# Optimization experiments

Hardware: AMD Instinct MI355X
Metric: run time of the kernel (lower is better)

Reference implementation:

```python
import jax, jax.numpy as jnp
import numpy as np

K = 12  # nsample_k; graph per point has K nodes (self + K-1 abs-diff neighbors)


def setup_inputs() -> dict:
    key = jax.random.key(0)
    k1, k2, k3 = jax.random.split(key, 3)
    p = jax.random.normal(k1, (2, 8192, 3), dtype=jnp.float32)
    W = jax.random.normal(k2, (1, 3), dtype=jnp.float32) * 0.5  # GCNConv lin weight [out=1, in=3]
    b = jax.random.normal(k3, (1,), dtype=jnp.float32) * 0.1    # GCNConv bias
    return {"p": p, "W": W, "b": b}


def _knn_idx(pts, k):
    # k nearest neighbors over the whole flattened cloud, self included then dropped
    pts = jax.lax.stop_gradient(pts)  # indices are non-differentiable
    sq = jnp.sum(pts * pts, axis=-1)                      # [n]
    d2 = sq[:, None] + sq[None, :] - 2.0 * (pts @ pts.T)  # [n, n] squared distances
    _, idx = jax.lax.top_k(-d2, k)                        # ascending distance
    return idx[:, 1:]                                     # drop self -> [n, k-1]


def reference(p, W, b):
    # p: [B, N, 3] -> flatten to [n, 3]
    pts = p.reshape(-1, 3)
    nidx = _knn_idx(pts, K)            # [n, K-1]
    nbr = pts[nidx]                    # [n, K-1, 3]
    # node features of each star graph: node 0 = point, nodes 1..K-1 = |p - neighbor|
    p_ij = jnp.concatenate([pts[:, None, :], jnp.abs(pts[:, None, :] - nbr)], axis=1)  # [n, K, 3]
    # GCNConv(3,1) on identical star graphs (edges 0->j, plus self loops), closed form:
    #   deg0 = 1, deg_j = 2  =>  out0 = x0 W^T + b ; out_j = x0 W^T / sqrt(2) + x_j W^T / 2 + b
    xw = jnp.einsum('nkc,oc->nko', p_ij, W)  # [n, K, 1]
    inv_s2 = 1.0 / jnp.sqrt(jnp.float32(2.0))
    out0 = xw[:, :1] + b                                  # [n, 1, 1]
    outj = inv_s2 * xw[:, :1] + 0.5 * xw[:, 1:] + b       # [n, K-1, 1]
    emb = jnp.concatenate([out0, outj], axis=1)           # [n, K, 1]
    # POOL: squeeze -> [n, K]; AdaptiveAvgPool1d(1) -> [n, 1]; module returns avg only
    return jnp.mean(emb[..., 0], axis=1, keepdims=True)   # [n, 1]
```

## Files before the change

### kernel.cpp

```cpp
#include <hip/hip_runtime.h>
#include <math.h>


#define NBINS  2048
#define PARTS  16
#define CMIN_  (-6.0f)
#define INVBW_ ((float)NBINS / 12.0f)
#define BLOCK  256
#define WPB    4
#define SEED   768
#define KK     12
#define CD     4
#define BIG    3.0e38f

__device__ __forceinline__ int bin_of(float x) {
  int b = (int)((x - CMIN_) * INVBW_);
  b = b < 0 ? 0 : b;
  b = b > NBINS - 1 ? NBINS - 1 : b;
  return b;
}

__device__ __forceinline__ float wave_min(float v) {
#pragma unroll
  for (int o = 1; o < 64; o <<= 1) v = fminf(v, __shfl_xor(v, o));
  return v;
}

__device__ __forceinline__ void ins4(float (&qd)[CD], float (&qw)[CD],
                                     float d, float w) {
#pragma unroll
  for (int k = CD - 1; k >= 1; --k) {
    const bool up  = (qd[k - 1] > d);
    const bool mid = (qd[k] > d);
    const float nd = up ? qd[k - 1] : (mid ? d : qd[k]);
    const float nw = up ? qw[k - 1] : (mid ? w : qw[k]);
    qd[k] = nd; qw[k] = nw;
  }
  if (qd[0] > d) { qw[0] = w; qd[0] = d; }
}

__global__ __launch_bounds__(1024)
void sort_kernel(const float* __restrict__ p, int* __restrict__ c_all,
                 float4* __restrict__ s_all, int n) {
  __shared__ int h_all[NBINS];
  __shared__ int h_pre[NBINS];
  __shared__ int wsum[16];
  const int tid  = threadIdx.x;
  const int dim  = blockIdx.x / PARTS;
  const int part = blockIdx.x % PARTS;
  const int chunk   = (n + PARTS - 1) / PARTS;
  const int myStart = part * chunk;
  const int myEnd   = min(myStart + chunk, n);

  h_all[tid] = 0; h_all[tid + 1024] = 0;
  h_pre[tid] = 0; h_pre[tid + 1024] = 0;
  __syncthreads();

  for (int i = tid; i < n; i += 1024) {
    const int b = bin_of(p[3 * i + dim]);
    atomicAdd(&h_all[b], 1);
    if (i < myStart) atomicAdd(&h_pre[b], 1);
  }
  __syncthreads();

  const int a = h_all[2 * tid], b = h_all[2 * tid + 1];
  const int v = a + b;
  const int lane = tid & 63, wid = tid >> 6;
  int incl = v;
#pragma unroll
  for (int o = 1; o < 64; o <<= 1) {
    const int t = __shfl_up(incl, o);
    if (lane >= o) incl += t;
  }
  if (lane == 63) wsum[wid] = incl;
  __syncthreads();
  int woff = 0;
  for (int wI = 0; wI < wid; ++wI) woff += wsum[wI];
  const int excl = woff + incl - v;

  if (part == 0) {
    int* __restrict__ cursor = c_all + (size_t)dim * NBINS;
    cursor[2 * tid]     = excl + a;
    cursor[2 * tid + 1] = excl + a + b;
  }

  const int c0 = excl + h_pre[2 * tid];
  const int c1 = excl + a + h_pre[2 * tid + 1];
  __syncthreads();
  h_pre[2 * tid]     = c0;
  h_pre[2 * tid + 1] = c1;
  __syncthreads();

  float4* __restrict__ sorted = s_all + (size_t)dim * n;
  for (int i = myStart + tid; i < myEnd; i += 1024) {
    const float x = p[3 * i], y = p[3 * i + 1], z = p[3 * i + 2];
    const float c = (dim == 0) ? x : (dim == 1) ? y : z;
    const int pos = atomicAdd(&h_pre[bin_of(c)], 1);
    sorted[pos] = make_float4(x, y, z, __int_as_float(i));
  }
}

__global__ __launch_bounds__(BLOCK, 1)
void query_kernel(const float4* __restrict__ sx, const float4* __restrict__ sy,
                  const float4* __restrict__ sz, const int* __restrict__ cx,
                  const int* __restrict__ cy, const int* __restrict__ cz,
                  const float* __restrict__ W, const float* __restrict__ bias,
                  float* __restrict__ out, int n) {
  const int lane = threadIdx.x & 63;
  const int wv   = threadIdx.x >> 6;
  const int t    = wv * (n >> 2) + blockIdx.x;
  const float W0 = W[0], W1 = W[1], W2 = W[2];
  const float bb = bias[0];

  const float4 me = sx[t];
  const float xi = me.x, yi = me.y, zi = me.z;
  const int orig = __float_as_int(me.w);

  const float ax = fabsf(xi), ay = fabsf(yi), az = fabsf(zi);
  const float4* sv; const int* cur; float cq;
  if (ay >= ax && ay >= az)      { sv = sy; cur = cy; cq = yi; }
  else if (az >= ax && az >= ay) { sv = sz; cur = cz; cq = zi; }
  else                           { sv = sx; cur = cx; cq = xi; }

  const int bq = bin_of(cq);
  const int bs = (bq > 0) ? cur[bq - 1] : 0;
  const int be = cur[bq];
  int lo = ((bs + be) >> 1) - SEED / 2;
  lo = lo < 0 ? 0 : lo;
  lo = lo > n - SEED ? n - SEED : lo;
  const float4* base = sv + lo + lane;

  float qd[CD], qw[CD];
  float ev = BIG;
#pragma unroll
  for (int k = 0; k < CD; ++k) { qd[k] = BIG; qw[k] = 0.f; }

#define PROCQ(cc, valid)                                                      \
  {                                                                           \
    const float dx = xi - (cc).x, dy = yi - (cc).y, dz = zi - (cc).z;         \
    float d2 = fmaf(dx, dx, fmaf(dy, dy, dz * dz));                           \
    d2 = (valid) ? d2 : BIG;                                                  \
    const float w = fmaf(W0, fabsf(dx), fmaf(W1, fabsf(dy), W2 * fabsf(dz))); \
    ev = fminf(ev, fmaxf(d2, qd[CD - 1]));                                    \
    ins4(qd, qw, d2, w);                                                      \
  }

  {
    float4 cs[SEED / 64];
#pragma unroll
    for (int s = 0; s < SEED / 64; ++s) cs[s] = base[s * 64];
    __builtin_amdgcn_sched_barrier(0);
#pragma unroll
    for (int s = 0; s < SEED / 64; ++s) PROCQ(cs[s], true)
  }

  float u;
  {
    const float m = qd[0];
    float hiv = m;
#pragma unroll
    for (int o = 1; o < 64; o <<= 1) hiv = fmaxf(hiv, __shfl_xor(hiv, o));
    float lov = 0.f;
#pragma unroll
    for (int it = 0; it < 10; ++it) {
      const float mid = 0.5f * (lov + hiv);
      const int cnt = __popcll(__ballot(m <= mid));
      if (cnt >= KK) hiv = mid; else lov = mid;
    }
    u = hiv;
  }

  const float s = sqrtf(u);
  const int bl = bin_of(cq - s);
  const int bh = bin_of(cq + s);
  const int lo2 = (bl > 0) ? cur[bl - 1] : 0;
  const int hi2 = cur[bh];
  const int steps = (hi2 - lo2 + 63) >> 6;

  {
    const int a0 = lo2, b0 = min(hi2, lo);
    const int len = b0 - a0;
    const int nch = (len + 63) >> 6;
    for (int c0 = 0; c0 < nch; ++c0) {
      const int idx = c0 * 64 + lane;
      const float4 c = sv[a0 + min(idx, len - 1)];
      PROCQ(c, idx < len)
    }
  }
  {
    const int a0 = max(lo2, lo + SEED), b0 = hi2;
    const int len = b0 - a0;
    const int nch = (len + 63) >> 6;
    for (int c0 = 0; c0 < nch; ++c0) {
      const int idx = c0 * 64 + lane;
      const float4 c = sv[a0 + min(idx, len - 1)];
      PROCQ(c, idx < len)
    }
  }
#undef PROCQ

  float acc = 0.f;
  float tau = 0.f;
#pragma unroll
  for (int r = 0; r < KK; ++r) {
    const float mm = wave_min(qd[0]);
    const unsigned long long bal = __ballot(qd[0] == mm);
    if (qd[0] == mm && lane == (int)(__ffsll(bal) - 1)) {
      acc += qw[0];
#pragma unroll
      for (int k = 0; k < CD - 1; ++k) { qd[k] = qd[k + 1]; qw[k] = qw[k + 1]; }
      qd[CD - 1] = BIG;
    }
    tau = mm;
  }

  const bool ovf = __ballot(ev <= tau) != 0ULL;
  if (ovf) {
    float dd[KK];
#pragma unroll
    for (int k = 0; k < KK; ++k) dd[k] = BIG;
    for (int s0 = 0; s0 < steps; ++s0) {
      const int pos = lo2 + s0 * 64 + lane;
      const float4 c = sv[(pos < hi2) ? pos : hi2 - 1];
      const float dx = xi - c.x, dy = yi - c.y, dz = zi - c.z;
      const float d2 = (pos < hi2) ? fmaf(dx, dx, fmaf(dy, dy, dz * dz)) : BIG;
#pragma unroll
      for (int k = KK - 1; k >= 1; --k)
        dd[k] = __builtin_amdgcn_fmed3f(d2, dd[k - 1], dd[k]);
      dd[0] = fminf(dd[0], d2);
    }
    float tau2 = 0.f;
#pragma unroll
    for (int r = 0; r < KK; ++r) {
      const float mm = wave_min(dd[0]);
      if (dd[0] == mm) {
#pragma unroll
        for (int k = 0; k < KK - 1; ++k) dd[k] = dd[k + 1];
        dd[KK - 1] = BIG;
      }
      tau2 = mm;
    }
    acc = 0.f;
    for (int s0 = 0; s0 < steps; ++s0) {
      const int pos = lo2 + s0 * 64 + lane;
      if (pos < hi2) {
        const float4 c = sv[pos];
        const float dx = xi - c.x, dy = yi - c.y, dz = zi - c.z;
        const float d2 = fmaf(dx, dx, fmaf(dy, dy, dz * dz));
        const float w  = fmaf(W0, fabsf(dx), fmaf(W1, fabsf(dy), W2 * fabsf(dz)));
        acc += (d2 <= tau2) ? w : 0.f;
      }
    }
  }

#pragma unroll
  for (int o = 1; o < 64; o <<= 1) acc += __shfl_xor(acc, o);
  if (lane == 0) {
    const float xw0 = W0 * xi + W1 * yi + W2 * zi;
    out[orig] = bb + (xw0 * 8.778174593052022f + 0.5f * acc) * (1.0f / 12.0f);
  }
}

extern "C" void kernel_launch(void* const* d_in, const int* in_sizes, int n_in,
                              void* d_out, int out_size, void* d_ws, size_t ws_size,
                              hipStream_t stream) {
  const float* p  = (const float*)d_in[0];
  const float* W  = (const float*)d_in[1];
  const float* bb = (const float*)d_in[2];
  float* out = (float*)d_out;

  const int n = in_sizes[0] / 3;

  int*    c_all = (int*)d_ws;
  float4* s_all = (float4*)((char*)d_ws + 3 * NBINS * 4);
  int*    cx = c_all;
  int*    cy = cx + NBINS;
  int*    cz = cy + NBINS;
  float4* sx = s_all;
  float4* sy = sx + n;
  float4* sz = sy + n;

  sort_kernel<<<3 * PARTS, 1024, 0, stream>>>(p, c_all, s_all, n);
  query_kernel<<<n / WPB, BLOCK, 0, stream>>>(sx, sy, sz, cx, cy, cz, W, bb, out, n);
}
```

Baseline: 109.6 us.

## Track only distances in per-lane queue, accumulate weights in a final threshold pass

The per-lane top-4 queue now holds only squared distances and is updated with fmed3 instead of a compare/select insert that also carried weights. The weighted sum is no longer gathered during selection. After the k-th distance threshold is found, a final pass over the candidate window re-reads points and sums weights for those within the threshold. The seed loads are also issued in groups of four without a scheduling barrier. This lowers ALU and register cost in the hot selection loop, but every wave now pays an extra full pass over the window instead of only overflowing waves.

```diff
diff --git a/kernel.cpp b/kernel.cpp
--- a/kernel.cpp
+++ b/kernel.cpp
@@ -24,19 +24,6 @@
 #pragma unroll
   for (int o = 1; o < 64; o <<= 1) v = fminf(v, __shfl_xor(v, o));
   return v;
-}
-
-__device__ __forceinline__ void ins4(float (&qd)[CD], float (&qw)[CD],
-                                     float d, float w) {
-#pragma unroll
-  for (int k = CD - 1; k >= 1; --k) {
-    const bool up  = (qd[k - 1] > d);
-    const bool mid = (qd[k] > d);
-    const float nd = up ? qd[k - 1] : (mid ? d : qd[k]);
-    const float nw = up ? qw[k - 1] : (mid ? w : qw[k]);
-    qd[k] = nd; qw[k] = nw;
-  }
-  if (qd[0] > d) { qw[0] = w; qd[0] = d; }
 }
 
 __global__ __launch_bounds__(1024)
@@ -130,33 +117,35 @@
   lo = lo > n - SEED ? n - SEED : lo;
   const float4* base = sv + lo + lane;
 
-  float qd[CD], qw[CD];
+  float dd[CD];
   float ev = BIG;
 #pragma unroll
-  for (int k = 0; k < CD; ++k) { qd[k] = BIG; qw[k] = 0.f; }
-
-#define PROCQ(cc, valid)                                                      \
+  for (int k = 0; k < CD; ++k) dd[k] = BIG;
+
+#define PROCD(cc, valid)                                                      \
   {                                                                           \
     const float dx = xi - (cc).x, dy = yi - (cc).y, dz = zi - (cc).z;         \
     float d2 = fmaf(dx, dx, fmaf(dy, dy, dz * dz));                           \
     d2 = (valid) ? d2 : BIG;                                                  \
-    const float w = fmaf(W0, fabsf(dx), fmaf(W1, fabsf(dy), W2 * fabsf(dz))); \
-    ev = fminf(ev, fmaxf(d2, qd[CD - 1]));                                    \
-    ins4(qd, qw, d2, w);                                                      \
-  }
-
-  {
-    float4 cs[SEED / 64];
-#pragma unroll
-    for (int s = 0; s < SEED / 64; ++s) cs[s] = base[s * 64];
-    __builtin_amdgcn_sched_barrier(0);
-#pragma unroll
-    for (int s = 0; s < SEED / 64; ++s) PROCQ(cs[s], true)
+    ev = fminf(ev, fmaxf(d2, dd[CD - 1]));                                    \
+    dd[3] = __builtin_amdgcn_fmed3f(d2, dd[2], dd[3]);                        \
+    dd[2] = __builtin_amdgcn_fmed3f(d2, dd[1], dd[2]);                        \
+    dd[1] = __builtin_amdgcn_fmed3f(d2, dd[0], dd[1]);                        \
+    dd[0] = fminf(dd[0], d2);                                                 \
+  }
+
+#pragma unroll
+  for (int s = 0; s < SEED / 64; s += 4) {
+    const float4 c0 = base[(s + 0) * 64];
+    const float4 c1 = base[(s + 1) * 64];
+    const float4 c2 = base[(s + 2) * 64];
+    const float4 c3 = base[(s + 3) * 64];
+    PROCD(c0, true) PROCD(c1, true) PROCD(c2, true) PROCD(c3, true)
   }
 
   float u;
   {
-    const float m = qd[0];
+    const float m = dd[0];
     float hiv = m;
 #pragma unroll
     for (int o = 1; o < 64; o <<= 1) hiv = fmaxf(hiv, __shfl_xor(hiv, o));
@@ -175,50 +164,46 @@
   const int bh = bin_of(cq + s);
   const int lo2 = (bl > 0) ? cur[bl - 1] : 0;
   const int hi2 = cur[bh];
-  const int steps = (hi2 - lo2 + 63) >> 6;
+  const int lenE  = hi2 - lo2;
+  const int steps = (lenE + 63) >> 6;
 
   {
     const int a0 = lo2, b0 = min(hi2, lo);
     const int len = b0 - a0;
     const int nch = (len + 63) >> 6;
-    for (int c0 = 0; c0 < nch; ++c0) {
-      const int idx = c0 * 64 + lane;
+    for (int c0i = 0; c0i < nch; ++c0i) {
+      const int idx = c0i * 64 + lane;
       const float4 c = sv[a0 + min(idx, len - 1)];
-      PROCQ(c, idx < len)
+      PROCD(c, idx < len)
     }
   }
   {
     const int a0 = max(lo2, lo + SEED), b0 = hi2;
     const int len = b0 - a0;
     const int nch = (len + 63) >> 6;
-    for (int c0 = 0; c0 < nch; ++c0) {
-      const int idx = c0 * 64 + lane;
+    for (int c0i = 0; c0i < nch; ++c0i) {
+      const int idx = c0i * 64 + lane;
       const float4 c = sv[a0 + min(idx, len - 1)];
-      PROCQ(c, idx < len)
-    }
-  }
-#undef PROCQ
-
-  float acc = 0.f;
+      PROCD(c, idx < len)
+    }
+  }
+#undef PROCD
+
   float tau = 0.f;
 #pragma unroll
   for (int r = 0; r < KK; ++r) {
-    const float mm = wave_min(qd[0]);
-    const unsigned long long bal = __ballot(qd[0] == mm);
-    if (qd[0] == mm && lane == (int)(__ffsll(bal) - 1)) {
-      acc += qw[0];
-#pragma unroll
-      for (int k = 0; k < CD - 1; ++k) { qd[k] = qd[k + 1]; qw[k] = qw[k + 1]; }
-      qd[CD - 1] = BIG;
+    const float mm = wave_min(dd[0]);
+    const unsigned long long bal = __ballot(dd[0] == mm);
+    if (dd[0] == mm && lane == (int)(__ffsll(bal) - 1)) {
+      dd[0] = dd[1]; dd[1] = dd[2]; dd[2] = dd[3]; dd[3] = BIG;
     }
     tau = mm;
   }
 
-  const bool ovf = __ballot(ev <= tau) != 0ULL;
-  if (ovf) {
-    float dd[KK];
-#pragma unroll
-    for (int k = 0; k < KK; ++k) dd[k] = BIG;
+  if (__ballot(ev <= tau) != 0ULL) {
+    float d12[KK];
+#pragma unroll
+    for (int k = 0; k < KK; ++k) d12[k] = BIG;
     for (int s0 = 0; s0 < steps; ++s0) {
       const int pos = lo2 + s0 * 64 + lane;
       const float4 c = sv[(pos < hi2) ? pos : hi2 - 1];
@@ -226,31 +211,30 @@
       const float d2 = (pos < hi2) ? fmaf(dx, dx, fmaf(dy, dy, dz * dz)) : BIG;
 #pragma unroll
       for (int k = KK - 1; k >= 1; --k)
-        dd[k] = __builtin_amdgcn_fmed3f(d2, dd[k - 1], dd[k]);
-      dd[0] = fminf(dd[0], d2);
-    }
-    float tau2 = 0.f;
+        d12[k] = __builtin_amdgcn_fmed3f(d2, d12[k - 1], d12[k]);
+      d12[0] = fminf(d12[0], d2);
+    }
+    tau = 0.f;
 #pragma unroll
     for (int r = 0; r < KK; ++r) {
-      const float mm = wave_min(dd[0]);
-      if (dd[0] == mm) {
-#pragma unroll
-        for (int k = 0; k < KK - 1; ++k) dd[k] = dd[k + 1];
-        dd[KK - 1] = BIG;
+      const float mm = wave_min(d12[0]);
+      if (d12[0] == mm) {
+#pragma unroll
+        for (int k = 0; k < KK - 1; ++k) d12[k] = d12[k + 1];
+        d12[KK - 1] = BIG;
       }
-      tau2 = mm;
-    }
-    acc = 0.f;
-    for (int s0 = 0; s0 < steps; ++s0) {
-      const int pos = lo2 + s0 * 64 + lane;
-      if (pos < hi2) {
-        const float4 c = sv[pos];
-        const float dx = xi - c.x, dy = yi - c.y, dz = zi - c.z;
-        const float d2 = fmaf(dx, dx, fmaf(dy, dy, dz * dz));
-        const float w  = fmaf(W0, fabsf(dx), fmaf(W1, fabsf(dy), W2 * fabsf(dz)));
-        acc += (d2 <= tau2) ? w : 0.f;
-      }
-    }
+      tau = mm;
+    }
+  }
+
+  float acc = 0.f;
+  for (int s0 = 0; s0 < steps; ++s0) {
+    const int idx = s0 * 64 + lane;
+    const float4 c = sv[lo2 + min(idx, lenE - 1)];
+    const float dx = xi - c.x, dy = yi - c.y, dz = zi - c.z;
+    const float d2 = fmaf(dx, dx, fmaf(dy, dy, dz * dz));
+    const float w  = fmaf(W0, fabsf(dx), fmaf(W1, fabsf(dy), W2 * fabsf(dz)));
+    acc += (d2 <= tau && idx < lenE) ? w : 0.f;
   }
 
 #pragma unroll
```

Result: no change. 109.7 us (+0.1%).
